# Performance work log

Measured on AMD Instinct MI355X. Metric: run time of the kernel, lower is better.

## Reference

```python
import jax, jax.numpy as jnp
import numpy as np

A, B, I, J, K = 8, 256, 256, 256, 256  # a=batch, b=tokens, i=s-channels, j=c-channels, k=out_dim


def setup_inputs() -> dict:
    key = jax.random.key(0)
    k1, k2, k3 = jax.random.split(key, 3)
    input_s = jax.random.normal(k1, (A, B, I), dtype=jnp.float32)
    input_c = jax.random.normal(k2, (B, J), dtype=jnp.float32)
    # learned params: w ~ N(0, 0.02), b zeros (as in build())
    w = jax.random.normal(k3, (I, J, K), dtype=jnp.float32) * 0.02
    b = jnp.zeros((K,), dtype=jnp.float32)
    return {"input_s": input_s, "input_c": input_c, "w": w, "b": b}


def reference(input_s, input_c, w, b):
    # Original: tmp = einsum('abi,ijk->abjk', input_s, w); out = einsum('bj,abjk->abk', input_c, tmp) + b
    # Mathematically identical fused bilinear contraction (avoids the [a,b,j,k] intermediate):
    out = jnp.einsum('abi,bj,ijk->abk', input_s, input_c, w)
    return out + b
```

## Files before the change

kernel.cpp:

```cpp
#include <hip/hip_runtime.h>
#include <hip/hip_bf16.h>

#define A_ 8
#define B_ 256
#define I_ 256
#define J_ 256
#define K_ 256

typedef __attribute__((ext_vector_type(8))) short short8_t;
typedef __attribute__((ext_vector_type(4))) float f32x4_t;
typedef __attribute__((ext_vector_type(4))) uint u32x4_t;

static __device__ __forceinline__ uint pack2bf(float a, float b) {
  float2 f2; f2.x = a; f2.y = b;
  __hip_bfloat162 h2 = __float22bfloat162_rn(f2);
  uint r;
  __builtin_memcpy(&r, &h2, 4);
  return r;
}

static __device__ __forceinline__ ushort f2bf(float f) {
  __hip_bfloat16 h = __float2bfloat16(f);
  ushort us;
  __builtin_memcpy(&us, &h, 2);
  return us;
}

static __device__ __forceinline__ float bf2f(ushort h) {
  uint u = ((uint)h) << 16;
  float f;
  __builtin_memcpy(&f, &u, 4);
  return f;
}

__global__ __launch_bounds__(256) void prepass_kernel(
    const float* __restrict__ c, ushort* __restrict__ cbf) {
  const int idx = blockIdx.x * 256 + threadIdx.x;
  const f32x4_t v = *reinterpret_cast<const f32x4_t*>(c + (size_t)idx * 4);
  uint2 r;
  r.x = pack2bf(v[0], v[1]);
  r.y = pack2bf(v[2], v[3]);
  *reinterpret_cast<uint2*>(cbf + (size_t)idx * 4) = r;
}

#define BK 32
#define LDB 40

__global__ __launch_bounds__(256, 2) void pass1_kernel(
    const ushort* __restrict__ cbf, const float* __restrict__ w,
    ushort* __restrict__ u) {
  const int i    = blockIdx.x;
  const int k0   = blockIdx.y * 64;
  const int tid  = threadIdx.x;
  const int lane = tid & 63;
  const int wave = tid >> 6;
  const int lrow = lane & 15;
  const int lhi  = lane >> 4;

  __shared__ ushort Bt[2][64][LDB];

  const float* wi = w + (size_t)i * (J_ * K_) + k0;

  const int bk = tid & 63;
  const int jb = (tid >> 6) * 8;

  const int arow = wave * 64 + lrow;

  f32x4_t acc[4][4];
#pragma unroll
  for (int m = 0; m < 4; m++)
#pragma unroll
    for (int n = 0; n < 4; n++) acc[m][n] = (f32x4_t)(0.0f);

  float    brg[2][8];
  short8_t afr[2][4];

#define LOADB(p, j0)                                                       \
  {                                                                        \
    const float* sb = wi + (size_t)((j0) + jb) * K_ + bk;                  \
    _Pragma("unroll") for (int q = 0; q < 8; q++)                          \
        brg[p][q] = sb[(size_t)q * K_];                                    \
  }
#define LOADA(p, j0)                                                       \
  {                                                                        \
    _Pragma("unroll") for (int m = 0; m < 4; m++)                          \
        afr[p][m] = *reinterpret_cast<const short8_t*>(                    \
            cbf + (size_t)(arow + m * 16) * J_ + (j0) + lhi * 8);          \
  }
#define STOREB(buf, p)                                                     \
  {                                                                        \
    u32x4_t t4;                                                            \
    _Pragma("unroll") for (int q = 0; q < 4; q++)                          \
        t4[q] = pack2bf(brg[p][2 * q], brg[p][2 * q + 1]);                 \
    *reinterpret_cast<u32x4_t*>(&Bt[buf][bk][jb]) = t4;                    \
  }

  LOADB(0, 0);
  LOADA(0, 0);
  STOREB(0, 0);
  __syncthreads();

#pragma unroll
  for (int t = 0; t < 8; ++t) {
    const int cur = t & 1;
    const int nxt = cur ^ 1;
    if (t < 7) {
      LOADB(nxt, (t + 1) * BK);
      LOADA(nxt, (t + 1) * BK);
    }
    short8_t bfr[4];
#pragma unroll
    for (int n = 0; n < 4; n++)
      bfr[n] = *reinterpret_cast<const short8_t*>(
          &Bt[cur][n * 16 + lrow][lhi * 8]);
#pragma unroll
    for (int m = 0; m < 4; m++)
#pragma unroll
      for (int n = 0; n < 4; n++)
        acc[m][n] = __builtin_amdgcn_mfma_f32_16x16x32_bf16(
            afr[cur][m], bfr[n], acc[m][n], 0, 0, 0);
    if (t < 7) STOREB(nxt, nxt);
    __syncthreads();
  }

#pragma unroll
  for (int m = 0; m < 4; m++) {
    const int brow = wave * 64 + m * 16 + lhi * 4;
#pragma unroll
    for (int n = 0; n < 4; n++) {
      const int kc = k0 + n * 16 + lrow;
      ushort* up = u + ((size_t)brow * I_ + i) * K_ + kc;
#pragma unroll
      for (int r = 0; r < 4; r++)
        up[(size_t)r * (I_ * K_)] = f2bf(acc[m][n][r]);
    }
  }
#undef LOADB
#undef LOADA
#undef STOREB
}

__global__ __launch_bounds__(256) void pass2_kernel(
    const float* __restrict__ s, const ushort* __restrict__ u,
    const float* __restrict__ bias, float* __restrict__ out) {
  const int b   = blockIdx.x;
  const int a0  = blockIdx.y * 4;
  const int tid = threadIdx.x;
  __shared__ float s_l[4][I_];
  __shared__ float red[8][4][K_];

#pragma unroll
  for (int v = 0; v < 4; v++) {
    const int idx = tid + v * 256;
    const int a = idx >> 8, ii = idx & 255;
    s_l[a][ii] = s[((size_t)(a0 + a) * B_ + b) * I_ + ii];
  }
  __syncthreads();

  const int kb = (tid & 31) * 8;
  const int ig = tid >> 5;
  float acc[4][8];
#pragma unroll
  for (int a = 0; a < 4; a++)
#pragma unroll
    for (int q = 0; q < 8; q++) acc[a][q] = 0.0f;

  const ushort* ub = u + ((size_t)b * I_ + ig * 32) * K_ + kb;
  for (int ii = 0; ii < 32; ++ii) {
    const short8_t uv = *reinterpret_cast<const short8_t*>(ub + (size_t)ii * K_);
    float f[8];
#pragma unroll
    for (int q = 0; q < 8; q++) f[q] = bf2f((ushort)uv[q]);
    const int i = ig * 32 + ii;
#pragma unroll
    for (int a = 0; a < 4; a++) {
      const float sa = s_l[a][i];
#pragma unroll
      for (int q = 0; q < 8; q++) acc[a][q] += sa * f[q];
    }
  }

#pragma unroll
  for (int a = 0; a < 4; a++) {
    f32x4_t r0, r1;
#pragma unroll
    for (int q = 0; q < 4; q++) { r0[q] = acc[a][q]; r1[q] = acc[a][4 + q]; }
    *reinterpret_cast<f32x4_t*>(&red[ig][a][kb])     = r0;
    *reinterpret_cast<f32x4_t*>(&red[ig][a][kb + 4]) = r1;
  }
  __syncthreads();

#pragma unroll
  for (int v = 0; v < 4; v++) {
    const int k = tid;
    float sum = 0.0f;
#pragma unroll
    for (int g = 0; g < 8; g++) sum += red[g][v][k];
    out[((size_t)(a0 + v) * B_ + b) * K_ + k] = sum + bias[k];
  }
}

__global__ __launch_bounds__(256) void fallback_kernel(
    const float* __restrict__ s, const float* __restrict__ cmat,
    const float* __restrict__ w, const float* __restrict__ bias,
    float* __restrict__ out) {
  const int b = blockIdx.x;
  const int k = threadIdx.x;
  __shared__ float c_l[J_];
  __shared__ float s_l[A_][I_];
  for (int idx = threadIdx.x; idx < J_; idx += 256) c_l[idx] = cmat[(size_t)b * J_ + idx];
  for (int idx = threadIdx.x; idx < A_ * I_; idx += 256) {
    const int a = idx >> 8;
    const int i = idx & 255;
    s_l[a][i] = s[(size_t)a * (B_ * I_) + (size_t)b * I_ + i];
  }
  __syncthreads();
  float acc[A_];
#pragma unroll
  for (int a = 0; a < A_; a++) acc[a] = 0.0f;
  for (int i = 0; i < I_; i++) {
    const float* wrow = w + (size_t)i * (J_ * K_) + k;
    float inner = 0.0f;
    for (int j = 0; j < J_; j++) inner += c_l[j] * wrow[(size_t)j * K_];
#pragma unroll
    for (int a = 0; a < A_; a++) acc[a] += s_l[a][i] * inner;
  }
#pragma unroll
  for (int a = 0; a < A_; a++)
    out[((size_t)a * B_ + b) * K_ + k] = acc[a] + bias[k];
}

extern "C" void kernel_launch(void* const* d_in, const int* in_sizes, int n_in,
                              void* d_out, int out_size, void* d_ws, size_t ws_size,
                              hipStream_t stream) {
  const float* s    = (const float*)d_in[0];
  const float* cmat = (const float*)d_in[1];
  const float* w    = (const float*)d_in[2];
  const float* bias = (const float*)d_in[3];
  float* out = (float*)d_out;

  const size_t u_elems = (size_t)B_ * I_ * K_;
  const size_t need = u_elems * sizeof(ushort) + (size_t)B_ * J_ * sizeof(ushort);
  if (ws_size >= need) {
    ushort* u   = (ushort*)d_ws;
    ushort* cbf = (ushort*)d_ws + u_elems;
    prepass_kernel<<<dim3((B_ * J_) / (256 * 4)), dim3(256), 0, stream>>>(cmat, cbf);
    pass1_kernel<<<dim3(I_, 4), dim3(256), 0, stream>>>(cbf, w, u);
    pass2_kernel<<<dim3(B_, 2), dim3(256), 0, stream>>>(s, u, bias, out);
  } else {
    fallback_kernel<<<dim3(B_), dim3(256), 0, stream>>>(s, cmat, w, bias, out);
  }
}
```

Measured before the change: 42.24 us.

## Interleave intermediate in groups of four tokens and retile pass2 around it

Pass1 now loads w with 16-byte vector reads instead of scalar strided loads. It writes the bf16 intermediate as packed 4-token groups, using one 8-byte store per MFMA output instead of four scattered 2-byte stores. Pass2 is retiled so each block handles 4 tokens and all 8 batches for 64 output columns, reading s into a transposed shared layout and reusing each u load across 32 accumulators. This targets uncoalesced global traffic in both passes. The cost is larger shared memory use in pass2 and some extra LDS transposition.

```diff
diff --git a/kernel.cpp b/kernel.cpp
--- a/kernel.cpp
+++ b/kernel.cpp
@@ -9,7 +9,6 @@
 
 typedef __attribute__((ext_vector_type(8))) short short8_t;
 typedef __attribute__((ext_vector_type(4))) float f32x4_t;
-typedef __attribute__((ext_vector_type(4))) uint u32x4_t;
 
 static __device__ __forceinline__ uint pack2bf(float a, float b) {
   float2 f2; f2.x = a; f2.y = b;
@@ -19,15 +18,7 @@
   return r;
 }
 
-static __device__ __forceinline__ ushort f2bf(float f) {
-  __hip_bfloat16 h = __float2bfloat16(f);
-  ushort us;
-  __builtin_memcpy(&us, &h, 2);
-  return us;
-}
-
-static __device__ __forceinline__ float bf2f(ushort h) {
-  uint u = ((uint)h) << 16;
+static __device__ __forceinline__ float bits2f(uint u) {
   float f;
   __builtin_memcpy(&f, &u, 4);
   return f;
@@ -44,11 +35,11 @@
 }
 
 #define BK 32
-#define LDB 40
+#define LDK 40
 
 __global__ __launch_bounds__(256, 2) void pass1_kernel(
     const ushort* __restrict__ cbf, const float* __restrict__ w,
-    ushort* __restrict__ u) {
+    ushort* __restrict__ u2) {
   const int i    = blockIdx.x;
   const int k0   = blockIdx.y * 64;
   const int tid  = threadIdx.x;
@@ -57,12 +48,12 @@
   const int lrow = lane & 15;
   const int lhi  = lane >> 4;
 
-  __shared__ ushort Bt[2][64][LDB];
+  __shared__ ushort Bt[2][64][LDK];
 
   const float* wi = w + (size_t)i * (J_ * K_) + k0;
 
-  const int bk = tid & 63;
-  const int jb = (tid >> 6) * 8;
+  const int jp = tid & 15;
+  const int kq = tid >> 4;
 
   const int arow = wave * 64 + lrow;
 
@@ -72,27 +63,26 @@
 #pragma unroll
     for (int n = 0; n < 4; n++) acc[m][n] = (f32x4_t)(0.0f);
 
-  float    brg[2][8];
+  f32x4_t  bv[2][2];
   short8_t afr[2][4];
 
-#define LOADB(p, j0)                                                       \
-  {                                                                        \
-    const float* sb = wi + (size_t)((j0) + jb) * K_ + bk;                  \
-    _Pragma("unroll") for (int q = 0; q < 8; q++)                          \
-        brg[p][q] = sb[(size_t)q * K_];                                    \
-  }
-#define LOADA(p, j0)                                                       \
-  {                                                                        \
-    _Pragma("unroll") for (int m = 0; m < 4; m++)                          \
-        afr[p][m] = *reinterpret_cast<const short8_t*>(                    \
-            cbf + (size_t)(arow + m * 16) * J_ + (j0) + lhi * 8);          \
-  }
-#define STOREB(buf, p)                                                     \
-  {                                                                        \
-    u32x4_t t4;                                                            \
-    _Pragma("unroll") for (int q = 0; q < 4; q++)                          \
-        t4[q] = pack2bf(brg[p][2 * q], brg[p][2 * q + 1]);                 \
-    *reinterpret_cast<u32x4_t*>(&Bt[buf][bk][jb]) = t4;                    \
+#define LOADB(p, j0)                                                        \
+  {                                                                         \
+    _Pragma("unroll") for (int jj = 0; jj < 2; jj++)                        \
+        bv[p][jj] = *reinterpret_cast<const f32x4_t*>(                      \
+            wi + (size_t)((j0) + jp * 2 + jj) * K_ + kq * 4);               \
+  }
+#define LOADA(p, j0)                                                        \
+  {                                                                         \
+    _Pragma("unroll") for (int m = 0; m < 4; m++)                           \
+        afr[p][m] = *reinterpret_cast<const short8_t*>(                     \
+            cbf + (size_t)(arow + m * 16) * J_ + (j0) + lhi * 8);           \
+  }
+#define STOREB(buf, p)                                                      \
+  {                                                                         \
+    _Pragma("unroll") for (int kk = 0; kk < 4; kk++)                        \
+        *reinterpret_cast<uint*>(&Bt[buf][kq * 4 + kk][jp * 2]) =           \
+            pack2bf(bv[p][0][kk], bv[p][1][kk]);                            \
   }
 
   LOADB(0, 0);
@@ -125,14 +115,15 @@
 
 #pragma unroll
   for (int m = 0; m < 4; m++) {
-    const int brow = wave * 64 + m * 16 + lhi * 4;
+    const int b4 = wave * 16 + m * 4 + lhi;
 #pragma unroll
     for (int n = 0; n < 4; n++) {
       const int kc = k0 + n * 16 + lrow;
-      ushort* up = u + ((size_t)brow * I_ + i) * K_ + kc;
-#pragma unroll
-      for (int r = 0; r < 4; r++)
-        up[(size_t)r * (I_ * K_)] = f2bf(acc[m][n][r]);
+      uint2 val;
+      val.x = pack2bf(acc[m][n][0], acc[m][n][1]);
+      val.y = pack2bf(acc[m][n][2], acc[m][n][3]);
+      *reinterpret_cast<uint2*>(
+          u2 + (((size_t)b4 * I_ + i) * K_ + kc) * 4) = val;
     }
   }
 #undef LOADB
@@ -141,62 +132,90 @@
 }
 
 __global__ __launch_bounds__(256) void pass2_kernel(
-    const float* __restrict__ s, const ushort* __restrict__ u,
+    const float* __restrict__ s, const ushort* __restrict__ u2,
     const float* __restrict__ bias, float* __restrict__ out) {
-  const int b   = blockIdx.x;
-  const int a0  = blockIdx.y * 4;
+  const int b4  = blockIdx.x;
+  const int kq  = blockIdx.y;
   const int tid = threadIdx.x;
-  __shared__ float s_l[4][I_];
-  __shared__ float red[8][4][K_];
-
-#pragma unroll
-  for (int v = 0; v < 4; v++) {
-    const int idx = tid + v * 256;
-    const int a = idx >> 8, ii = idx & 255;
-    s_l[a][ii] = s[((size_t)(a0 + a) * B_ + b) * I_ + ii];
-  }
-  __syncthreads();
-
-  const int kb = (tid & 31) * 8;
-  const int ig = tid >> 5;
-  float acc[4][8];
-#pragma unroll
-  for (int a = 0; a < 4; a++)
-#pragma unroll
-    for (int q = 0; q < 8; q++) acc[a][q] = 0.0f;
-
-  const ushort* ub = u + ((size_t)b * I_ + ig * 32) * K_ + kb;
-  for (int ii = 0; ii < 32; ++ii) {
-    const short8_t uv = *reinterpret_cast<const short8_t*>(ub + (size_t)ii * K_);
-    float f[8];
-#pragma unroll
-    for (int q = 0; q < 8; q++) f[q] = bf2f((ushort)uv[q]);
-    const int i = ig * 32 + ii;
-#pragma unroll
-    for (int a = 0; a < 4; a++) {
-      const float sa = s_l[a][i];
-#pragma unroll
-      for (int q = 0; q < 8; q++) acc[a][q] += sa * f[q];
-    }
-  }
-
-#pragma unroll
-  for (int a = 0; a < 4; a++) {
-    f32x4_t r0, r1;
-#pragma unroll
-    for (int q = 0; q < 4; q++) { r0[q] = acc[a][q]; r1[q] = acc[a][4 + q]; }
-    *reinterpret_cast<f32x4_t*>(&red[ig][a][kb])     = r0;
-    *reinterpret_cast<f32x4_t*>(&red[ig][a][kb + 4]) = r1;
-  }
-  __syncthreads();
-
-#pragma unroll
-  for (int v = 0; v < 4; v++) {
-    const int k = tid;
-    float sum = 0.0f;
-#pragma unroll
-    for (int g = 0; g < 8; g++) sum += red[g][v][k];
-    out[((size_t)(a0 + v) * B_ + b) * K_ + k] = sum + bias[k];
+  const int kl  = tid & 63;
+  const int ig  = tid >> 6;
+  const int k   = kq * 64 + kl;
+
+  __shared__ float smem[256 * 32];
+
+  {
+    const int pair = tid >> 3;
+    const int a    = pair >> 2;
+    const int rb   = pair & 3;
+    const int ic   = (tid & 7) * 32;
+    const float* src = s + ((size_t)a * B_ + b4 * 4 + rb) * I_ + ic;
+#pragma unroll
+    for (int q = 0; q < 8; q++) {
+      const f32x4_t v = *reinterpret_cast<const f32x4_t*>(src + q * 4);
+#pragma unroll
+      for (int e = 0; e < 4; e++)
+        smem[(ic + q * 4 + e) * 32 + rb * 8 + a] = v[e];
+    }
+  }
+  __syncthreads();
+
+  float acc[8][4];
+#pragma unroll
+  for (int a = 0; a < 8; a++)
+#pragma unroll
+    for (int rb = 0; rb < 4; rb++) acc[a][rb] = 0.0f;
+
+  const ushort* ubase = u2 + (((size_t)b4 * I_ + ig * 64) * K_ + k) * 4;
+#pragma unroll 4
+  for (int ii = 0; ii < 64; ++ii) {
+    const uint2 uv =
+        *reinterpret_cast<const uint2*>(ubase + (size_t)ii * (K_ * 4));
+    float uf[4];
+    uf[0] = bits2f(uv.x << 16);
+    uf[1] = bits2f(uv.x & 0xffff0000u);
+    uf[2] = bits2f(uv.y << 16);
+    uf[3] = bits2f(uv.y & 0xffff0000u);
+    const float* srow = &smem[(ig * 64 + ii) * 32];
+#pragma unroll
+    for (int rb = 0; rb < 4; rb++) {
+      const f32x4_t s0 = *reinterpret_cast<const f32x4_t*>(srow + rb * 8);
+      const f32x4_t s1 = *reinterpret_cast<const f32x4_t*>(srow + rb * 8 + 4);
+#pragma unroll
+      for (int e = 0; e < 4; e++) {
+        acc[e][rb]     += s0[e] * uf[rb];
+        acc[4 + e][rb] += s1[e] * uf[rb];
+      }
+    }
+  }
+  __syncthreads();
+
+  {
+    float* dst = &smem[(ig * 64 + kl) * 32];
+#pragma unroll
+    for (int a = 0; a < 8; a++) {
+      f32x4_t v;
+#pragma unroll
+      for (int rb = 0; rb < 4; rb++) v[rb] = acc[a][rb];
+      *reinterpret_cast<f32x4_t*>(dst + a * 4) = v;
+    }
+  }
+  __syncthreads();
+
+  {
+    const int kl2 = tid & 63;
+    const int pr  = tid >> 6;
+    const int kk  = kq * 64 + kl2;
+    const float bk = bias[kk];
+#pragma unroll
+    for (int q = 0; q < 8; q++) {
+      const int p = pr * 8 + q;
+      float sum = 0.0f;
+#pragma unroll
+      for (int g = 0; g < 4; g++) sum += smem[((g * 64) + kl2) * 32 + p];
+      const int a  = p >> 2;
+      const int rb = p & 3;
+      out[((size_t)a * B_ + b4 * 4 + rb) * K_ + kk] = sum + bk;
+    }
   }
 }
 
@@ -242,11 +261,11 @@
   const size_t u_elems = (size_t)B_ * I_ * K_;
   const size_t need = u_elems * sizeof(ushort) + (size_t)B_ * J_ * sizeof(ushort);
   if (ws_size >= need) {
-    ushort* u   = (ushort*)d_ws;
+    ushort* u2  = (ushort*)d_ws;
     ushort* cbf = (ushort*)d_ws + u_elems;
     prepass_kernel<<<dim3((B_ * J_) / (256 * 4)), dim3(256), 0, stream>>>(cmat, cbf);
-    pass1_kernel<<<dim3(I_, 4), dim3(256), 0, stream>>>(cbf, w, u);
-    pass2_kernel<<<dim3(B_, 2), dim3(256), 0, stream>>>(s, u, bias, out);
+    pass1_kernel<<<dim3(I_, 4), dim3(256), 0, stream>>>(cbf, w, u2);
+    pass2_kernel<<<dim3(64, 4), dim3(256), 0, stream>>>(s, u2, bias, out);
   } else {
     fallback_kernel<<<dim3(B_), dim3(256), 0, stream>>>(s, cmat, w, bias, out);
   }
```

New measurement: 67.80 us. 60.5% more time.

## Pre-transpose weights to bf16 K-major layout and load MFMA operands directly

Applied to the files above, without the earlier changes.

Adds a prepass kernel that converts w to bf16 and transposes it so J is contiguous for each (i,k). This lets pass1 load both MFMA operands straight from global memory, with no LDS staging and no barriers. When the workspace is too small for the transposed copy, a mid path keeps the LDS kernel but switches its w loads to float4 vectors. The cost is an extra full pass over w on every call: read 64MB, write a 32MB bf16 copy, then read that copy again in pass1.

```diff
diff --git a/kernel.cpp b/kernel.cpp
--- a/kernel.cpp
+++ b/kernel.cpp
@@ -33,7 +33,7 @@
   return f;
 }
 
-__global__ __launch_bounds__(256) void prepass_kernel(
+__global__ __launch_bounds__(256) void prepass_c_kernel(
     const float* __restrict__ c, ushort* __restrict__ cbf) {
   const int idx = blockIdx.x * 256 + threadIdx.x;
   const f32x4_t v = *reinterpret_cast<const f32x4_t*>(c + (size_t)idx * 4);
@@ -43,10 +43,107 @@
   *reinterpret_cast<uint2*>(cbf + (size_t)idx * 4) = r;
 }
 
-#define BK 32
-#define LDB 40
+__global__ __launch_bounds__(256, 2) void prepass_w_kernel(
+    const float* __restrict__ w, ushort* __restrict__ wt) {
+  const int i   = blockIdx.x;
+  const int tid = threadIdx.x;
+  const int jp  = tid & 15;
+  const int ks  = tid >> 4;
+  __shared__ uint T[256][17];
+
+  const float* wi  = w  + (size_t)i * (J_ * K_);
+  ushort*      wti = wt + (size_t)i * (J_ * K_);
+
+  for (int jc = 0; jc < 8; ++jc) {
+    const int j = jc * 32 + jp * 2;
+    f32x4_t r0[4], r1[4];
+#pragma unroll
+    for (int q = 0; q < 4; q++) {
+      r0[q] = *reinterpret_cast<const f32x4_t*>(wi + (size_t)j * K_ + ks * 16 + q * 4);
+      r1[q] = *reinterpret_cast<const f32x4_t*>(wi + (size_t)(j + 1) * K_ + ks * 16 + q * 4);
+    }
+    if (jc) __syncthreads();
+#pragma unroll
+    for (int q = 0; q < 4; q++)
+#pragma unroll
+      for (int e = 0; e < 4; e++)
+        T[ks * 16 + q * 4 + e][jp] = pack2bf(r0[q][e], r1[q][e]);
+    __syncthreads();
+    uint row[16];
+#pragma unroll
+    for (int p = 0; p < 16; p++) row[p] = T[tid][p];
+#pragma unroll
+    for (int q = 0; q < 4; q++) {
+      u32x4_t v;
+#pragma unroll
+      for (int e = 0; e < 4; e++) v[e] = row[q * 4 + e];
+      *reinterpret_cast<u32x4_t*>(wti + (size_t)tid * J_ + jc * 32 + q * 8) = v;
+    }
+  }
+}
 
 __global__ __launch_bounds__(256, 2) void pass1_kernel(
+    const ushort* __restrict__ cbf, const ushort* __restrict__ wt,
+    ushort* __restrict__ u) {
+  const int i    = blockIdx.x;
+  const int k0   = blockIdx.y * 64;
+  const int tid  = threadIdx.x;
+  const int lane = tid & 63;
+  const int wave = tid >> 6;
+  const int lrow = lane & 15;
+  const int lhi  = lane >> 4;
+
+  const ushort* wtik = wt + ((size_t)i * K_ + k0) * J_;
+  const int arow = wave * 64 + lrow;
+
+  f32x4_t acc[4][4];
+#pragma unroll
+  for (int m = 0; m < 4; m++)
+#pragma unroll
+    for (int n = 0; n < 4; n++) acc[m][n] = (f32x4_t)(0.0f);
+
+  short8_t af[2][4], bfr[2][4];
+
+#define LOADSTEP(p, j0)                                                     \
+  {                                                                         \
+    _Pragma("unroll") for (int m = 0; m < 4; m++)                           \
+        af[p][m] = *reinterpret_cast<const short8_t*>(                      \
+            cbf + (size_t)(arow + m * 16) * J_ + (j0) + lhi * 8);           \
+    _Pragma("unroll") for (int n = 0; n < 4; n++)                           \
+        bfr[p][n] = *reinterpret_cast<const short8_t*>(                     \
+            wtik + (size_t)(n * 16 + lrow) * J_ + (j0) + lhi * 8);          \
+  }
+
+  LOADSTEP(0, 0);
+#pragma unroll
+  for (int t = 0; t < 8; ++t) {
+    const int cur = t & 1;
+    if (t < 7) LOADSTEP(cur ^ 1, (t + 1) * 32);
+#pragma unroll
+    for (int m = 0; m < 4; m++)
+#pragma unroll
+      for (int n = 0; n < 4; n++)
+        acc[m][n] = __builtin_amdgcn_mfma_f32_16x16x32_bf16(
+            af[cur][m], bfr[cur][n], acc[m][n], 0, 0, 0);
+  }
+#undef LOADSTEP
+
+#pragma unroll
+  for (int m = 0; m < 4; m++) {
+    const int brow = wave * 64 + m * 16 + lhi * 4;
+#pragma unroll
+    for (int n = 0; n < 4; n++) {
+      const int kc = k0 + n * 16 + lrow;
+      ushort* up = u + ((size_t)brow * I_ + i) * K_ + kc;
+#pragma unroll
+      for (int r = 0; r < 4; r++)
+        up[(size_t)r * (I_ * K_)] = f2bf(acc[m][n][r]);
+    }
+  }
+}
+
+#define LDK 40
+__global__ __launch_bounds__(256, 2) void pass1_lds_kernel(
     const ushort* __restrict__ cbf, const float* __restrict__ w,
     ushort* __restrict__ u) {
   const int i    = blockIdx.x;
@@ -57,13 +154,10 @@
   const int lrow = lane & 15;
   const int lhi  = lane >> 4;
 
-  __shared__ ushort Bt[2][64][LDB];
-
+  __shared__ ushort Bt[2][64][LDK];
   const float* wi = w + (size_t)i * (J_ * K_) + k0;
-
-  const int bk = tid & 63;
-  const int jb = (tid >> 6) * 8;
-
+  const int jp = tid & 15;
+  const int kq = tid >> 4;
   const int arow = wave * 64 + lrow;
 
   f32x4_t acc[4][4];
@@ -72,27 +166,26 @@
 #pragma unroll
     for (int n = 0; n < 4; n++) acc[m][n] = (f32x4_t)(0.0f);
 
-  float    brg[2][8];
-  short8_t afr[2][4];
-
-#define LOADB(p, j0)                                                       \
-  {                                                                        \
-    const float* sb = wi + (size_t)((j0) + jb) * K_ + bk;                  \
-    _Pragma("unroll") for (int q = 0; q < 8; q++)                          \
-        brg[p][q] = sb[(size_t)q * K_];                                    \
-  }
-#define LOADA(p, j0)                                                       \
-  {                                                                        \
-    _Pragma("unroll") for (int m = 0; m < 4; m++)                          \
-        afr[p][m] = *reinterpret_cast<const short8_t*>(                    \
-            cbf + (size_t)(arow + m * 16) * J_ + (j0) + lhi * 8);          \
-  }
-#define STOREB(buf, p)                                                     \
-  {                                                                        \
-    u32x4_t t4;                                                            \
-    _Pragma("unroll") for (int q = 0; q < 4; q++)                          \
-        t4[q] = pack2bf(brg[p][2 * q], brg[p][2 * q + 1]);                 \
-    *reinterpret_cast<u32x4_t*>(&Bt[buf][bk][jb]) = t4;                    \
+  f32x4_t  bv[2][2];
+  short8_t af[2][4];
+
+#define LOADB(p, j0)                                                        \
+  {                                                                         \
+    _Pragma("unroll") for (int jj = 0; jj < 2; jj++)                        \
+        bv[p][jj] = *reinterpret_cast<const f32x4_t*>(                      \
+            wi + (size_t)((j0) + jp * 2 + jj) * K_ + kq * 4);               \
+  }
+#define LOADA(p, j0)                                                        \
+  {                                                                         \
+    _Pragma("unroll") for (int m = 0; m < 4; m++)                           \
+        af[p][m] = *reinterpret_cast<const short8_t*>(                      \
+            cbf + (size_t)(arow + m * 16) * J_ + (j0) + lhi * 8);           \
+  }
+#define STOREB(buf, p)                                                      \
+  {                                                                         \
+    _Pragma("unroll") for (int kk = 0; kk < 4; kk++)                        \
+        *reinterpret_cast<uint*>(&Bt[buf][kq * 4 + kk][jp * 2]) =           \
+            pack2bf(bv[p][0][kk], bv[p][1][kk]);                            \
   }
 
   LOADB(0, 0);
@@ -105,8 +198,8 @@
     const int cur = t & 1;
     const int nxt = cur ^ 1;
     if (t < 7) {
-      LOADB(nxt, (t + 1) * BK);
-      LOADA(nxt, (t + 1) * BK);
+      LOADB(nxt, (t + 1) * 32);
+      LOADA(nxt, (t + 1) * 32);
     }
     short8_t bfr[4];
 #pragma unroll
@@ -118,7 +211,7 @@
 #pragma unroll
       for (int n = 0; n < 4; n++)
         acc[m][n] = __builtin_amdgcn_mfma_f32_16x16x32_bf16(
-            afr[cur][m], bfr[n], acc[m][n], 0, 0, 0);
+            af[cur][m], bfr[n], acc[m][n], 0, 0, 0);
     if (t < 7) STOREB(nxt, nxt);
     __syncthreads();
   }
@@ -239,13 +332,25 @@
   const float* bias = (const float*)d_in[3];
   float* out = (float*)d_out;
 
-  const size_t u_elems = (size_t)B_ * I_ * K_;
-  const size_t need = u_elems * sizeof(ushort) + (size_t)B_ * J_ * sizeof(ushort);
-  if (ws_size >= need) {
+  const size_t u_elems  = (size_t)B_ * I_ * K_;
+  const size_t wt_elems = (size_t)I_ * J_ * K_;
+  const size_t cbf_elems = (size_t)B_ * J_;
+  const size_t need_full = (u_elems + wt_elems + cbf_elems) * sizeof(ushort);
+  const size_t need_mid  = (u_elems + cbf_elems) * sizeof(ushort);
+
+  if (ws_size >= need_full) {
+    ushort* u   = (ushort*)d_ws;
+    ushort* wt  = (ushort*)d_ws + u_elems;
+    ushort* cbf = (ushort*)d_ws + u_elems + wt_elems;
+    prepass_c_kernel<<<dim3((B_ * J_) / (256 * 4)), dim3(256), 0, stream>>>(cmat, cbf);
+    prepass_w_kernel<<<dim3(I_), dim3(256), 0, stream>>>(w, wt);
+    pass1_kernel<<<dim3(I_, 4), dim3(256), 0, stream>>>(cbf, wt, u);
+    pass2_kernel<<<dim3(B_, 2), dim3(256), 0, stream>>>(s, u, bias, out);
+  } else if (ws_size >= need_mid) {
     ushort* u   = (ushort*)d_ws;
     ushort* cbf = (ushort*)d_ws + u_elems;
-    prepass_kernel<<<dim3((B_ * J_) / (256 * 4)), dim3(256), 0, stream>>>(cmat, cbf);
-    pass1_kernel<<<dim3(I_, 4), dim3(256), 0, stream>>>(cbf, w, u);
+    prepass_c_kernel<<<dim3((B_ * J_) / (256 * 4)), dim3(256), 0, stream>>>(cmat, cbf);
+    pass1_lds_kernel<<<dim3(I_, 4), dim3(256), 0, stream>>>(cbf, w, u);
     pass2_kernel<<<dim3(B_, 2), dim3(256), 0, stream>>>(s, u, bias, out);
   } else {
     fallback_kernel<<<dim3(B_), dim3(256), 0, stream>>>(s, cmat, w, bias, out);
```

Result: slower. 74.79 us (+77.0%).

## Deepen pass1 W prefetch to two stages with vectorized loads

Applied to the files above, without the earlier changes.

Pass1 now loads W with 16-byte float4 global loads (two j rows per thread) instead of eight scalar strided loads. It prefetches two K-steps ahead rather than one and replaces __syncthreads with an LDS-only waitcnt plus a raw barrier, so global loads can stay in flight across iterations. Launch bounds are raised to three blocks per SM to improve latency hiding. The trade-offs are more register pressure under the tighter occupancy bound and narrower 4-byte LDS stores that may bank-conflict.

```diff
diff --git a/kernel.cpp b/kernel.cpp
--- a/kernel.cpp
+++ b/kernel.cpp
@@ -9,7 +9,6 @@
 
 typedef __attribute__((ext_vector_type(8))) short short8_t;
 typedef __attribute__((ext_vector_type(4))) float f32x4_t;
-typedef __attribute__((ext_vector_type(4))) uint u32x4_t;
 
 static __device__ __forceinline__ uint pack2bf(float a, float b) {
   float2 f2; f2.x = a; f2.y = b;
@@ -33,7 +32,7 @@
   return f;
 }
 
-__global__ __launch_bounds__(256) void prepass_kernel(
+__global__ __launch_bounds__(256) void prepass_c_kernel(
     const float* __restrict__ c, ushort* __restrict__ cbf) {
   const int idx = blockIdx.x * 256 + threadIdx.x;
   const f32x4_t v = *reinterpret_cast<const f32x4_t*>(c + (size_t)idx * 4);
@@ -43,10 +42,9 @@
   *reinterpret_cast<uint2*>(cbf + (size_t)idx * 4) = r;
 }
 
-#define BK 32
-#define LDB 40
-
-__global__ __launch_bounds__(256, 2) void pass1_kernel(
+#define LDK 40
+
+__global__ __launch_bounds__(256, 3) void pass1_kernel(
     const ushort* __restrict__ cbf, const float* __restrict__ w,
     ushort* __restrict__ u) {
   const int i    = blockIdx.x;
@@ -57,12 +55,12 @@
   const int lrow = lane & 15;
   const int lhi  = lane >> 4;
 
-  __shared__ ushort Bt[2][64][LDB];
+  __shared__ ushort Bt[2][64][LDK];
 
   const float* wi = w + (size_t)i * (J_ * K_) + k0;
 
-  const int bk = tid & 63;
-  const int jb = (tid >> 6) * 8;
+  const int jp = tid & 15;
+  const int kq = tid >> 4;
 
   const int arow = wave * 64 + lrow;
 
@@ -72,56 +70,61 @@
 #pragma unroll
     for (int n = 0; n < 4; n++) acc[m][n] = (f32x4_t)(0.0f);
 
-  float    brg[2][8];
+  f32x4_t  bv[2][2];
   short8_t afr[2][4];
 
-#define LOADB(p, j0)                                                       \
-  {                                                                        \
-    const float* sb = wi + (size_t)((j0) + jb) * K_ + bk;                  \
-    _Pragma("unroll") for (int q = 0; q < 8; q++)                          \
-        brg[p][q] = sb[(size_t)q * K_];                                    \
-  }
-#define LOADA(p, j0)                                                       \
-  {                                                                        \
-    _Pragma("unroll") for (int m = 0; m < 4; m++)                          \
-        afr[p][m] = *reinterpret_cast<const short8_t*>(                    \
-            cbf + (size_t)(arow + m * 16) * J_ + (j0) + lhi * 8);          \
-  }
-#define STOREB(buf, p)                                                     \
-  {                                                                        \
-    u32x4_t t4;                                                            \
-    _Pragma("unroll") for (int q = 0; q < 4; q++)                          \
-        t4[q] = pack2bf(brg[p][2 * q], brg[p][2 * q + 1]);                 \
-    *reinterpret_cast<u32x4_t*>(&Bt[buf][bk][jb]) = t4;                    \
-  }
-
-  LOADB(0, 0);
-  LOADA(0, 0);
+#define BGLOB(p, t)                                                         \
+  {                                                                         \
+    _Pragma("unroll") for (int jj = 0; jj < 2; jj++)                        \
+        bv[p][jj] = *reinterpret_cast<const f32x4_t*>(                      \
+            wi + (size_t)((t) * 32 + jp * 2 + jj) * K_ + kq * 4);           \
+  }
+#define ALOAD(p, t)                                                         \
+  {                                                                         \
+    _Pragma("unroll") for (int m = 0; m < 4; m++)                           \
+        afr[p][m] = *reinterpret_cast<const short8_t*>(                     \
+            cbf + (size_t)(arow + m * 16) * J_ + (t) * 32 + lhi * 8);       \
+  }
+#define STOREB(buf, p)                                                      \
+  {                                                                         \
+    _Pragma("unroll") for (int kk = 0; kk < 4; kk++)                        \
+        *reinterpret_cast<uint*>(&Bt[buf][kq * 4 + kk][jp * 2]) =           \
+            pack2bf(bv[p][0][kk], bv[p][1][kk]);                            \
+  }
+
+  BGLOB(0, 0);
+  BGLOB(1, 1);
+  ALOAD(0, 0);
+  ALOAD(1, 1);
   STOREB(0, 0);
-  __syncthreads();
+  asm volatile("s_waitcnt lgkmcnt(0)" ::: "memory");
+  __builtin_amdgcn_s_barrier();
 
 #pragma unroll
   for (int t = 0; t < 8; ++t) {
     const int cur = t & 1;
-    const int nxt = cur ^ 1;
-    if (t < 7) {
-      LOADB(nxt, (t + 1) * BK);
-      LOADA(nxt, (t + 1) * BK);
-    }
     short8_t bfr[4];
 #pragma unroll
     for (int n = 0; n < 4; n++)
       bfr[n] = *reinterpret_cast<const short8_t*>(
           &Bt[cur][n * 16 + lrow][lhi * 8]);
+    if (t < 6) BGLOB(cur, t + 2);
 #pragma unroll
     for (int m = 0; m < 4; m++)
 #pragma unroll
       for (int n = 0; n < 4; n++)
         acc[m][n] = __builtin_amdgcn_mfma_f32_16x16x32_bf16(
             afr[cur][m], bfr[n], acc[m][n], 0, 0, 0);
-    if (t < 7) STOREB(nxt, nxt);
-    __syncthreads();
-  }
+    if (t < 6) ALOAD(cur, t + 2);
+    if (t < 7) {
+      STOREB(cur ^ 1, cur ^ 1);
+      asm volatile("s_waitcnt lgkmcnt(0)" ::: "memory");
+      __builtin_amdgcn_s_barrier();
+    }
+  }
+#undef BGLOB
+#undef ALOAD
+#undef STOREB
 
 #pragma unroll
   for (int m = 0; m < 4; m++) {
@@ -135,9 +138,6 @@
         up[(size_t)r * (I_ * K_)] = f2bf(acc[m][n][r]);
     }
   }
-#undef LOADB
-#undef LOADA
-#undef STOREB
 }
 
 __global__ __launch_bounds__(256) void pass2_kernel(
@@ -239,12 +239,14 @@
   const float* bias = (const float*)d_in[3];
   float* out = (float*)d_out;
 
-  const size_t u_elems = (size_t)B_ * I_ * K_;
-  const size_t need = u_elems * sizeof(ushort) + (size_t)B_ * J_ * sizeof(ushort);
+  const size_t u_elems   = (size_t)B_ * I_ * K_;
+  const size_t cbf_elems = (size_t)B_ * J_;
+  const size_t need = (u_elems + cbf_elems) * sizeof(ushort);
+
   if (ws_size >= need) {
     ushort* u   = (ushort*)d_ws;
     ushort* cbf = (ushort*)d_ws + u_elems;
-    prepass_kernel<<<dim3((B_ * J_) / (256 * 4)), dim3(256), 0, stream>>>(cmat, cbf);
+    prepass_c_kernel<<<dim3((B_ * J_) / (256 * 4)), dim3(256), 0, stream>>>(cmat, cbf);
     pass1_kernel<<<dim3(I_, 4), dim3(256), 0, stream>>>(cbf, w, u);
     pass2_kernel<<<dim3(B_, 2), dim3(256), 0, stream>>>(s, u, bias, out);
   } else {
```

Measured after the change: 46.83 us. 10.9% more time.
